# Kernel optimization log

Hardware: AMD Instinct MI355X
Metric: run time of the kernel (lower is better)

## Reference

```python
import jax, jax.numpy as jnp
import numpy as np

B, LQ, LK = 2, 2048, 77
DIM, XDIM = 320, 768
H, HD = 8, 40  # heads, head_dim; DIM == H*HD
FF = 4 * DIM  # GEGLU inner dim


def _ln(x, g, b, eps=1e-5):
    m = x.mean(-1, keepdims=True)
    v = ((x - m) ** 2).mean(-1, keepdims=True)
    return (x - m) * jax.lax.rsqrt(v + eps) * g + b


def _split_heads(x):  # [B,L,DIM] -> [B,H,L,HD]
    return x.reshape(x.shape[0], x.shape[1], H, HD).transpose(0, 2, 1, 3)


def _merge_heads(x):  # [B,H,L,HD] -> [B,L,DIM]
    return x.transpose(0, 2, 1, 3).reshape(x.shape[0], x.shape[2], H * HD)


def setup_inputs() -> dict:
    key = jax.random.key(0)
    ks = jax.random.split(key, 24)
    s = 0.02
    r = lambda i, shp: s * jax.random.normal(ks[i], shp, jnp.float32)
    return {
        "hidden_states": jax.random.normal(ks[0], (B, LQ, DIM), jnp.float32),
        "encoder_hidden_states": jax.random.normal(ks[1], (B, LK, XDIM), jnp.float32),
        # norm1 + self-attn (attn1)
        "ln1_g": jnp.ones((DIM,), jnp.float32), "ln1_b": jnp.zeros((DIM,), jnp.float32),
        "wq1": r(2, (DIM, DIM)), "wk1": r(3, (DIM, DIM)), "wv1": r(4, (DIM, DIM)),
        "wo1": r(5, (DIM, DIM)), "bo1": jnp.zeros((DIM,), jnp.float32),
        # norm2 + Hadamard cross-attn (attn2)
        "ln2_g": jnp.ones((DIM,), jnp.float32), "ln2_b": jnp.zeros((DIM,), jnp.float32),
        "wq2": r(6, (DIM, DIM)), "wk2": r(7, (XDIM, DIM)), "wvh": r(8, (DIM, DIM)),
        "wo2": r(9, (DIM, DIM)), "bo2": jnp.zeros((DIM,), jnp.float32),
        # norm3 + GEGLU feed-forward
        "ln3_g": jnp.ones((DIM,), jnp.float32), "ln3_b": jnp.zeros((DIM,), jnp.float32),
        "wff1": r(10, (DIM, 2 * FF)), "bff1": jnp.zeros((2 * FF,), jnp.float32),
        "wff2": r(11, (FF, DIM)), "bff2": jnp.zeros((DIM,), jnp.float32),
    }


def reference(hidden_states, encoder_hidden_states, ln1_g, ln1_b, wq1, wk1, wv1,
              wo1, bo1, ln2_g, ln2_b, wq2, wk2, wvh, wo2, bo2, ln3_g, ln3_b,
              wff1, bff1, wff2, bff2):
    scale = 1.0 / jnp.sqrt(jnp.asarray(HD, hidden_states.dtype))

    # ---- self-attention (SDPA semantics) ----
    h = _ln(hidden_states, ln1_g, ln1_b)
    q = _split_heads(h @ wq1)
    k = _split_heads(h @ wk1)
    v = _split_heads(h @ wv1)
    scores = jnp.einsum('bhqd,bhkd->bhqk', q, k) * scale
    w = jax.nn.softmax(scores, axis=-1)
    attn = jnp.einsum('bhqk,bhkd->bhqd', w, v)
    attn = _merge_heads(attn) @ wo1 + bo1
    hidden_states = hidden_states + attn

    # ---- Hadamard cross-attention: value comes from hidden_states (len Lq) ----
    h = _ln(hidden_states, ln2_g, ln2_b)
    q = _split_heads(h @ wq2)                     # [B,H,Lq,HD]
    k = _split_heads(encoder_hidden_states @ wk2) # [B,H,Lk,HD]
    vH = _split_heads(h @ wvh)                    # [B,H,Lq,HD]
    scores = jnp.einsum('bhqd,bhkd->bhqk', q, k) * scale
    w = jax.nn.softmax(scores, axis=-1)           # [B,H,Lq,Lk]
    # (w[...,None] * vH[...,None,:]).sum(-2) == vH * w.sum(-1, keepdims) (v indep of k)
    cross = vH * jnp.sum(w, axis=-1, keepdims=True)
    cross = _merge_heads(cross) @ wo2 + bo2
    hidden_states = hidden_states + cross

    # ---- GEGLU feed-forward ----
    h = _ln(hidden_states, ln3_g, ln3_b)
    proj = h @ wff1 + bff1
    x, gate = jnp.split(proj, 2, axis=-1)
    ff = (x * jax.nn.gelu(gate, approximate=False)) @ wff2 + bff2
    return hidden_states + ff
```

## Files before the change

kernel.cpp:

```cpp
#include <hip/hip_runtime.h>
#include <math.h>

#define DIM   320
#define HD    40
#define NH    8
#define LQ    2048
#define BATCH 2
#define MROWS 4096
#define FFD   1280
#define FF2   2560

#define KSPLIT 2
#define KCHUNK (LQ/KSPLIT)
#define KT     32
#define NT     (KCHUNK/KT)
#define NQROWS (BATCH*NH*LQ)

#define LSCALE (0.15811388300841897f * 1.4426950408889634f)

typedef unsigned short ushort_t;
typedef unsigned int u32;
using bf16x8 = __attribute__((ext_vector_type(8))) short;
using f32x4  = __attribute__((ext_vector_type(4))) float;

#define AS1 __attribute__((address_space(1)))
#define AS3 __attribute__((address_space(3)))

static __device__ inline ushort_t f2bf(float f) {
  union { float f; unsigned u; } x{f};
  unsigned r = x.u + 0x7FFFu + ((x.u >> 16) & 1u);
  return (ushort_t)(r >> 16);
}
static __device__ inline float bf2f(ushort_t h) {
  union { unsigned u; float f; } x; x.u = ((unsigned)h) << 16; return x.f;
}

#define OFF_WQKVT 0
#define OFF_WO1T  (960*320)
#define OFF_WO2T  (OFF_WO1T + 320*320)
#define OFF_WFF1T (OFF_WO2T + 320*320)
#define OFF_WFF2T (OFF_WFF1T + 320*2560)
#define OFF_WVHB  (OFF_WFF2T + 1280*320)
#define WBF_TOTAL (OFF_WVHB + 320*320)

__global__ __launch_bounds__(256) void convw_kernel(
    const float* __restrict__ wq1, const float* __restrict__ wk1,
    const float* __restrict__ wv1, const float* __restrict__ wo1,
    const float* __restrict__ wo2, const float* __restrict__ wff1,
    const float* __restrict__ wff2, const float* __restrict__ wvh,
    ushort_t* __restrict__ dst, ushort_t* __restrict__ Kimg,
    const float* __restrict__ hidden, const float* __restrict__ ln1_g,
    const float* __restrict__ ln1_b, ushort_t* __restrict__ lnb)
{
  int e = blockIdx.y;
  if (e == 8) {
    int f = blockIdx.x*256 + threadIdx.x;
    if (f < 98304) {
      int g3 = f/3, cidx = f - 3*g3;
      int rr = g3 & 31, tile = (g3 >> 5) & 63, bh = g3 >> 11;
      uint4 z = {0,0,0,0};
      *(uint4*)(Kimg + ((size_t)(bh*64 + tile))*2048 + rr*64
                + (((5+cidx) ^ (rr&7)) << 3)) = z;
    }
    return;
  }
  if (e == 9) {
    int row  = blockIdx.x * 4 + (threadIdx.x >> 6);
    int lane = threadIdx.x & 63;
    const float* x = hidden + (size_t)row * DIM;
    float v[5];
    float s = 0.f;
#pragma unroll
    for (int i = 0; i < 5; ++i) { v[i] = x[lane + 64*i]; s += v[i]; }
#pragma unroll
    for (int off = 32; off >= 1; off >>= 1) s += __shfl_xor(s, off, 64);
    float mean = s * (1.0f/DIM);
    float sq = 0.f;
#pragma unroll
    for (int i = 0; i < 5; ++i) { float d = v[i] - mean; sq += d*d; }
#pragma unroll
    for (int off = 32; off >= 1; off >>= 1) sq += __shfl_xor(sq, off, 64);
    float rstd = rsqrtf(sq*(1.0f/DIM) + 1e-5f);
    ushort_t* y = lnb + (size_t)row * DIM;
#pragma unroll
    for (int i = 0; i < 5; ++i) {
      int c = lane + 64*i;
      y[c] = f2bf((v[i]-mean)*rstd*ln1_g[c] + ln1_b[c]);
    }
    return;
  }
  const float* src; int K, N; size_t doff; int tr = 1; float scale = 1.f;
  switch (e) {
    case 0: src=wq1;  K=320;  N=320;  doff=OFF_WQKVT; scale=LSCALE; break;
    case 1: src=wk1;  K=320;  N=320;  doff=OFF_WQKVT + 320*320;  break;
    case 2: src=wv1;  K=320;  N=320;  doff=OFF_WQKVT + 2*320*320;break;
    case 3: src=wo1;  K=320;  N=320;  doff=OFF_WO1T;             break;
    case 4: src=wo2;  K=320;  N=320;  doff=OFF_WO2T;             break;
    case 5: src=wff1; K=320;  N=2560; doff=OFF_WFF1T;            break;
    case 6: src=wff2; K=1280; N=320;  doff=OFF_WFF2T;            break;
    default: src=wvh; K=320;  N=320;  doff=OFF_WVHB; tr=0;       break;
  }
  int ntN = N/32;
  int nt_total = (K/32)*ntN;
  int t = blockIdx.x;
  if (t >= nt_total) return;
  int kt = t / ntN, nt = t - kt*ntN;
  __shared__ float tile[32][33];
  int tx = threadIdx.x & 31, ty = threadIdx.x >> 5;
  ushort_t* d = dst + doff;
#pragma unroll
  for (int i = 0; i < 4; ++i) {
    int r = ty + 8*i;
    tile[r][tx] = src[(size_t)(kt*32+r)*N + nt*32+tx] * scale;
  }
  __syncthreads();
  if (tr) {
#pragma unroll
    for (int i = 0; i < 4; ++i) {
      int r = ty + 8*i;
      d[(size_t)(nt*32+r)*K + kt*32+tx] = f2bf(tile[tx][r]);
    }
  } else {
#pragma unroll
    for (int i = 0; i < 4; ++i) {
      int r = ty + 8*i;
      d[(size_t)(kt*32+r)*N + nt*32+tx] = f2bf(tile[r][tx]);
    }
  }
}

#define AST 72
__global__ __launch_bounds__(256) void mgemm(
    const ushort_t* __restrict__ A, int lda,
    const ushort_t* __restrict__ Bt, int ldb,
    const float* __restrict__ bias,
    const float* __restrict__ R,
    float* __restrict__ Cf, ushort_t* __restrict__ Cb, int ldc,
    int K)
{
  __shared__ ushort_t As[64*AST];
  __shared__ ushort_t Bs[64*AST];
  int tid = threadIdx.x;
  int w = tid >> 6, lane = tid & 63, quad = lane >> 4, n16 = lane & 15;
  int wm = w >> 1, wn = w & 1;
  int bm = blockIdx.y * 64, bn = blockIdx.x * 64;
  int sr = tid >> 2, sc = (tid & 3) << 4;
  const ushort_t* Ag = A  + (size_t)(bm + sr)*lda + sc;
  const ushort_t* Bg = Bt + (size_t)(bn + sr)*ldb + sc;

  f32x4 acc00 = {0.f,0.f,0.f,0.f}, acc01 = acc00, acc10 = acc00, acc11 = acc00;

  float4 av0 = *(const float4*)(Ag);
  float4 av1 = *(const float4*)(Ag + 8);
  float4 bv0 = *(const float4*)(Bg);
  float4 bv1 = *(const float4*)(Bg + 8);
  for (int k0 = 0; k0 < K; k0 += 64) {
    __syncthreads();
    *(float4*)(As + sr*AST + sc)     = av0;
    *(float4*)(As + sr*AST + sc + 8) = av1;
    *(float4*)(Bs + sr*AST + sc)     = bv0;
    *(float4*)(Bs + sr*AST + sc + 8) = bv1;
    __syncthreads();
    if (k0 + 64 < K) {
      av0 = *(const float4*)(Ag + k0 + 64);
      av1 = *(const float4*)(Ag + k0 + 72);
      bv0 = *(const float4*)(Bg + k0 + 64);
      bv1 = *(const float4*)(Bg + k0 + 72);
    }
#pragma unroll
    for (int kk = 0; kk < 64; kk += 32) {
      bf16x8 fa0 = *(const bf16x8*)(As + (wm*32 +      n16)*AST + kk + quad*8);
      bf16x8 fa1 = *(const bf16x8*)(As + (wm*32 + 16 + n16)*AST + kk + quad*8);
      bf16x8 fb0 = *(const bf16x8*)(Bs + (wn*32 +      n16)*AST + kk + quad*8);
      bf16x8 fb1 = *(const bf16x8*)(Bs + (wn*32 + 16 + n16)*AST + kk + quad*8);
      acc00 = __builtin_amdgcn_mfma_f32_16x16x32_bf16(fa0, fb0, acc00, 0,0,0);
      acc01 = __builtin_amdgcn_mfma_f32_16x16x32_bf16(fa0, fb1, acc01, 0,0,0);
      acc10 = __builtin_amdgcn_mfma_f32_16x16x32_bf16(fa1, fb0, acc10, 0,0,0);
      acc11 = __builtin_amdgcn_mfma_f32_16x16x32_bf16(fa1, fb1, acc11, 0,0,0);
    }
  }

  f32x4 accs[2][2] = {{acc00, acc01},{acc10, acc11}};
#pragma unroll
  for (int s = 0; s < 2; ++s)
#pragma unroll
    for (int t = 0; t < 2; ++t) {
      int c = bn + wn*32 + t*16 + n16;
      float bb = bias ? bias[c] : 0.f;
#pragma unroll
      for (int i = 0; i < 4; ++i) {
        int r = bm + wm*32 + s*16 + quad*4 + i;
        float v = accs[s][t][i] + bb;
        if (R)  v += R[(size_t)r*ldc + c];
        if (Cf) Cf[(size_t)r*ldc + c] = v;
        if (Cb) Cb[(size_t)r*ldc + c] = f2bf(v);
      }
    }
}

__global__ __launch_bounds__(256) void wc_gemm(
    const ushort_t* __restrict__ A, const ushort_t* __restrict__ Bt,
    ushort_t* __restrict__ Wctb)
{
  __shared__ ushort_t As[64*AST];
  __shared__ ushort_t Bs[64*AST];
  int tid = threadIdx.x;
  int w = tid >> 6, lane = tid & 63, quad = lane >> 4, n16 = lane & 15;
  int wm = w >> 1, wn = w & 1;
  int bm = blockIdx.y * 64, bn = blockIdx.x * 64;
  int sr = tid >> 2, sc = (tid & 3) << 4;
  const ushort_t* Ag = A  + (size_t)(bm + sr)*DIM + sc;
  const ushort_t* Bg = Bt + (size_t)(bn + sr)*DIM + sc;

  f32x4 acc00 = {0.f,0.f,0.f,0.f}, acc01 = acc00, acc10 = acc00, acc11 = acc00;

  float4 av0 = *(const float4*)(Ag);
  float4 av1 = *(const float4*)(Ag + 8);
  float4 bv0 = *(const float4*)(Bg);
  float4 bv1 = *(const float4*)(Bg + 8);
  for (int k0 = 0; k0 < DIM; k0 += 64) {
    __syncthreads();
    *(float4*)(As + sr*AST + sc)     = av0;
    *(float4*)(As + sr*AST + sc + 8) = av1;
    *(float4*)(Bs + sr*AST + sc)     = bv0;
    *(float4*)(Bs + sr*AST + sc + 8) = bv1;
    __syncthreads();
    if (k0 + 64 < DIM) {
      av0 = *(const float4*)(Ag + k0 + 64);
      av1 = *(const float4*)(Ag + k0 + 72);
      bv0 = *(const float4*)(Bg + k0 + 64);
      bv1 = *(const float4*)(Bg + k0 + 72);
    }
#pragma unroll
    for (int kk = 0; kk < 64; kk += 32) {
      bf16x8 fa0 = *(const bf16x8*)(As + (wm*32 +      n16)*AST + kk + quad*8);
      bf16x8 fa1 = *(const bf16x8*)(As + (wm*32 + 16 + n16)*AST + kk + quad*8);
      bf16x8 fb0 = *(const bf16x8*)(Bs + (wn*32 +      n16)*AST + kk + quad*8);
      bf16x8 fb1 = *(const bf16x8*)(Bs + (wn*32 + 16 + n16)*AST + kk + quad*8);
      acc00 = __builtin_amdgcn_mfma_f32_16x16x32_bf16(fa0, fb0, acc00, 0,0,0);
      acc01 = __builtin_amdgcn_mfma_f32_16x16x32_bf16(fa0, fb1, acc01, 0,0,0);
      acc10 = __builtin_amdgcn_mfma_f32_16x16x32_bf16(fa1, fb0, acc10, 0,0,0);
      acc11 = __builtin_amdgcn_mfma_f32_16x16x32_bf16(fa1, fb1, acc11, 0,0,0);
    }
  }

  f32x4 accs[2][2] = {{acc00, acc01},{acc10, acc11}};
#pragma unroll
  for (int s = 0; s < 2; ++s)
#pragma unroll
    for (int t = 0; t < 2; ++t) {
      int c = bn + wn*32 + t*16 + n16;
#pragma unroll
      for (int i = 0; i < 4; ++i) {
        int r = bm + wm*32 + s*16 + quad*4 + i;
        Wctb[((size_t)(c >> 5)*320 + r)*32
             + ((((c >> 3) & 3) ^ (r & 3)) << 3) + (c & 7)] = f2bf(accs[s][t][i]);
      }
    }
}

__global__ __launch_bounds__(256) void cross_ln(
    const float* __restrict__ h1,
    const float* __restrict__ g2, const float* __restrict__ b2,
    const ushort_t* __restrict__ Wctb,
    const float* __restrict__ bo2,
    const float* __restrict__ g3, const float* __restrict__ b3,
    float* __restrict__ h2, ushort_t* __restrict__ lnb)
{
  __shared__ ushort_t Asm[16*328];
  __shared__ ushort_t Bsm[2*10240];
  __shared__ float    sred[4][16][2];
  __shared__ float    fstat[16][2];
  int tid = threadIdx.x;
  int w = tid >> 6, lane = tid & 63, quad = lane >> 4, n16 = lane & 15;
  int r0 = blockIdx.x * 16;

  int ar = tid >> 4;
  int aj = tid & 15;
  {
    const float* hrow = h1 + (size_t)(r0 + ar)*DIM + aj*20;
    float xv[20];
    float s = 0.f, q = 0.f;
#pragma unroll
    for (int i = 0; i < 5; ++i) {
      float4 v = *(const float4*)(hrow + 4*i);
      xv[4*i]=v.x; xv[4*i+1]=v.y; xv[4*i+2]=v.z; xv[4*i+3]=v.w;
      s += v.x+v.y+v.z+v.w;
      q += v.x*v.x+v.y*v.y+v.z*v.z+v.w*v.w;
    }
#pragma unroll
    for (int off = 1; off < 16; off <<= 1) {
      s += __shfl_xor(s, off, 64);
      q += __shfl_xor(q, off, 64);
    }
    float m_  = s*(1.f/DIM);
    float rs_ = rsqrtf(fmaxf(q*(1.f/DIM) - m_*m_, 0.f) + 1e-5f);
    float gg[20], bb[20];
#pragma unroll
    for (int i = 0; i < 5; ++i) {
      *(float4*)(gg+4*i) = *(const float4*)(g2 + aj*20 + 4*i);
      *(float4*)(bb+4*i) = *(const float4*)(b2 + aj*20 + 4*i);
    }
    ushort_t tb[20];
#pragma unroll
    for (int j = 0; j < 20; ++j)
      tb[j] = f2bf((xv[j]-m_)*rs_*gg[j] + bb[j]);
#pragma unroll
    for (int i = 0; i < 5; ++i)
      *(uint2*)(Asm + ar*328 + aj*20 + 4*i) = *(uint2*)(tb + 4*i);
  }

#define STAGEB(BUF, KB) { \
  const ushort_t* src_ = Wctb + (size_t)(KB)*10240; \
  _Pragma("unroll") \
  for (int i = 0; i < 5; ++i) { \
    __builtin_amdgcn_global_load_lds( \
        (const AS1 u32*)(src_ + i*2048 + w*512 + lane*8), \
        (AS3 u32*)(Bsm + (BUF)*10240 + i*2048 + w*512), 16, 0, 0); \
  } }

  f32x4 acc[5];
#pragma unroll
  for (int t = 0; t < 5; ++t) acc[t] = f32x4{0.f,0.f,0.f,0.f};

  STAGEB(0, 0);
  __syncthreads();
  int bbuf = 0;
  for (int kb = 0; kb < 10; ++kb) {
    if (kb + 1 < 10) STAGEB(bbuf^1, kb + 1);
    const ushort_t* Bb = Bsm + bbuf*10240;
    bf16x8 fa = *(const bf16x8*)(Asm + n16*328 + kb*32 + quad*8);
#pragma unroll
    for (int t = 0; t < 5; ++t) {
      int c = w*80 + t*16 + n16;
      bf16x8 fb = *(const bf16x8*)(Bb + c*32 + ((quad ^ (c & 3)) << 3));
      acc[t] = __builtin_amdgcn_mfma_f32_16x16x32_bf16(fa, fb, acc[t], 0,0,0);
    }
    __syncthreads();
    bbuf ^= 1;
  }
#undef STAGEB

  float hv[5][4];
  float ss[4] = {0,0,0,0}, qq[4] = {0,0,0,0};
#pragma unroll
  for (int t = 0; t < 5; ++t) {
    int c = w*80 + t*16 + n16;
    float bb = bo2[c];
#pragma unroll
    for (int i = 0; i < 4; ++i) {
      int r = r0 + quad*4 + i;
      float v = acc[t][i] + bb + h1[(size_t)r*DIM + c];
      hv[t][i] = v;
      h2[(size_t)r*DIM + c] = v;
      ss[i] += v; qq[i] += v*v;
    }
  }
#pragma unroll
  for (int off = 1; off < 16; off <<= 1)
#pragma unroll
    for (int i = 0; i < 4; ++i) {
      ss[i] += __shfl_xor(ss[i], off, 64);
      qq[i] += __shfl_xor(qq[i], off, 64);
    }
  if (n16 == 0)
#pragma unroll
    for (int i = 0; i < 4; ++i) {
      sred[w][quad*4 + i][0] = ss[i];
      sred[w][quad*4 + i][1] = qq[i];
    }
  __syncthreads();
  if (tid < 16) {
    float S = sred[0][tid][0]+sred[1][tid][0]+sred[2][tid][0]+sred[3][tid][0];
    float Q = sred[0][tid][1]+sred[1][tid][1]+sred[2][tid][1]+sred[3][tid][1];
    float mm = S*(1.f/DIM);
    fstat[tid][0] = mm;
    fstat[tid][1] = rsqrtf(fmaxf(Q*(1.f/DIM) - mm*mm, 0.f) + 1e-5f);
  }
  __syncthreads();
#pragma unroll
  for (int t = 0; t < 5; ++t) {
    int c = w*80 + t*16 + n16;
    float gg = g3[c], bb = b3[c];
#pragma unroll
    for (int i = 0; i < 4; ++i) {
      int rr = quad*4 + i;
      lnb[(size_t)(r0 + rr)*DIM + c] =
          f2bf((hv[t][i] - fstat[rr][0])*fstat[rr][1]*gg + bb);
    }
  }
}

__global__ __launch_bounds__(256) void mgemm128_qkv(
    const ushort_t* __restrict__ A, const ushort_t* __restrict__ Bt,
    ushort_t* __restrict__ Qb, ushort_t* __restrict__ Kimg,
    ushort_t* __restrict__ Vimg)
{
  __shared__ ushort_t As[128*AST];
  __shared__ ushort_t Bs[64*AST];
  int tid = threadIdx.x;
  int w = tid >> 6, lane = tid & 63, quad = lane >> 4, n16 = lane & 15;
  int wm = w >> 1, wn = w & 1;
  int bm = blockIdx.y * 128, bn = blockIdx.x * 64;
  int ar = tid >> 2, ac = (tid & 3) << 4;
  const ushort_t* Ag0 = A  + (size_t)(bm + ar)*DIM + ac;
  const ushort_t* Ag1 = A  + (size_t)(bm + 64 + ar)*DIM + ac;
  const ushort_t* Bg  = Bt + (size_t)(bn + ar)*DIM + ac;

  f32x4 acc[4][2];
#pragma unroll
  for (int s = 0; s < 4; ++s)
#pragma unroll
    for (int t = 0; t < 2; ++t) acc[s][t] = f32x4{0.f,0.f,0.f,0.f};

  float4 a00 = *(const float4*)(Ag0);
  float4 a01 = *(const float4*)(Ag0 + 8);
  float4 a10 = *(const float4*)(Ag1);
  float4 a11 = *(const float4*)(Ag1 + 8);
  float4 b0  = *(const float4*)(Bg);
  float4 b1  = *(const float4*)(Bg + 8);
  for (int k0 = 0; k0 < DIM; k0 += 64) {
    __syncthreads();
    *(float4*)(As + ar*AST + ac)          = a00;
    *(float4*)(As + ar*AST + ac + 8)      = a01;
    *(float4*)(As + (64+ar)*AST + ac)     = a10;
    *(float4*)(As + (64+ar)*AST + ac + 8) = a11;
    *(float4*)(Bs + ar*AST + ac)          = b0;
    *(float4*)(Bs + ar*AST + ac + 8)      = b1;
    __syncthreads();
    if (k0 + 64 < DIM) {
      a00 = *(const float4*)(Ag0 + k0 + 64);
      a01 = *(const float4*)(Ag0 + k0 + 72);
      a10 = *(const float4*)(Ag1 + k0 + 64);
      a11 = *(const float4*)(Ag1 + k0 + 72);
      b0  = *(const float4*)(Bg  + k0 + 64);
      b1  = *(const float4*)(Bg  + k0 + 72);
    }
#pragma unroll
    for (int kk = 0; kk < 64; kk += 32) {
      bf16x8 fa[4], fb[2];
#pragma unroll
      for (int s = 0; s < 4; ++s)
        fa[s] = *(const bf16x8*)(As + (wm*64 + s*16 + n16)*AST + kk + quad*8);
#pragma unroll
      for (int t = 0; t < 2; ++t)
        fb[t] = *(const bf16x8*)(Bs + (wn*32 + t*16 + n16)*AST + kk + quad*8);
#pragma unroll
      for (int s = 0; s < 4; ++s)
#pragma unroll
        for (int t = 0; t < 2; ++t)
          acc[s][t] = __builtin_amdgcn_mfma_f32_16x16x32_bf16(fa[s], fb[t], acc[s][t], 0,0,0);
    }
  }

  int b8 = (bm >> 11) << 3;
  if (bn < 320) {
#pragma unroll
    for (int s = 0; s < 4; ++s)
#pragma unroll
      for (int t = 0; t < 2; ++t) {
        int c = bn + wn*32 + t*16 + n16;
#pragma unroll
        for (int i = 0; i < 4; ++i) {
          int r = bm + wm*64 + s*16 + quad*4 + i;
          Qb[(size_t)r*320 + c] = f2bf(acc[s][t][i]);
        }
      }
  } else if (bn < 640) {
#pragma unroll
    for (int t = 0; t < 2; ++t) {
      int c = bn + wn*32 + t*16 + n16 - 320;
      int hK = c / 40, d = c - hK*40;
#pragma unroll
      for (int s = 0; s < 4; ++s)
#pragma unroll
        for (int i = 0; i < 4; ++i) {
          int r = bm + wm*64 + s*16 + quad*4 + i;
          int l = r & 2047, tl = l >> 5, rr = l & 31;
          Kimg[((size_t)((b8 + hK)*64 + tl))*2048 + rr*64
               + (((d >> 3) ^ (rr & 7)) << 3) + (d & 7)] = f2bf(acc[s][t][i]);
        }
    }
  } else {
#pragma unroll
    for (int t = 0; t < 2; ++t) {
      int c = bn + wn*32 + t*16 + n16 - 640;
      int hV = c / 40, d = c - hV*40;
#pragma unroll
      for (int s = 0; s < 4; ++s) {
        int l0 = (bm + wm*64 + s*16 + quad*4) & 2047;
        int tl = l0 >> 5, p0 = (l0 & 31) >> 1;
        ushort_t* vb = Vimg + ((size_t)((b8 + hV)*64 + tl))*1536 + d*32;
#pragma unroll
        for (int j = 0; j < 2; ++j) {
          int p = p0 + j;
          unsigned val = (unsigned)f2bf(acc[s][t][2*j])
                       | ((unsigned)f2bf(acc[s][t][2*j+1]) << 16);
          *(unsigned*)(vb + (((p >> 2) ^ (d & 3)) << 3) + ((p & 3) << 1)) = val;
        }
      }
    }
  }
}

__global__ __launch_bounds__(256) void ff1_geglu(
    const ushort_t* __restrict__ A, const ushort_t* __restrict__ Bt,
    const float* __restrict__ bias, ushort_t* __restrict__ Og)
{
  __shared__ ushort_t As[128*AST];
  __shared__ ushort_t Bxs[64*AST];
  __shared__ ushort_t Bgs[64*AST];
  int tid = threadIdx.x;
  int w = tid >> 6, lane = tid & 63, quad = lane >> 4, n16 = lane & 15;
  int wm = w >> 1, wn = w & 1;
  int bm = blockIdx.y * 128, bn = blockIdx.x * 64;
  int ar = tid >> 2, ac = (tid & 3) << 4;
  const ushort_t* Ag0 = A  + (size_t)(bm + ar)*DIM + ac;
  const ushort_t* Ag1 = A  + (size_t)(bm + 64 + ar)*DIM + ac;
  const ushort_t* Bxg = Bt + (size_t)(bn + ar)*DIM + ac;
  const ushort_t* Bgg = Bt + (size_t)(bn + FFD + ar)*DIM + ac;

  f32x4 ax[4][2], ag[4][2];
#pragma unroll
  for (int s = 0; s < 4; ++s)
#pragma unroll
    for (int t = 0; t < 2; ++t) { ax[s][t] = f32x4{0.f,0.f,0.f,0.f}; ag[s][t] = ax[s][t]; }

  float4 a00 = *(const float4*)(Ag0);
  float4 a01 = *(const float4*)(Ag0 + 8);
  float4 a10 = *(const float4*)(Ag1);
  float4 a11 = *(const float4*)(Ag1 + 8);
  float4 bx0 = *(const float4*)(Bxg);
  float4 bx1 = *(const float4*)(Bxg + 8);
  float4 bg0 = *(const float4*)(Bgg);
  float4 bg1 = *(const float4*)(Bgg + 8);
  for (int k0 = 0; k0 < DIM; k0 += 64) {
    __syncthreads();
    *(float4*)(As  + ar*AST + ac)          = a00;
    *(float4*)(As  + ar*AST + ac + 8)      = a01;
    *(float4*)(As  + (64+ar)*AST + ac)     = a10;
    *(float4*)(As  + (64+ar)*AST + ac + 8) = a11;
    *(float4*)(Bxs + ar*AST + ac)          = bx0;
    *(float4*)(Bxs + ar*AST + ac + 8)      = bx1;
    *(float4*)(Bgs + ar*AST + ac)          = bg0;
    *(float4*)(Bgs + ar*AST + ac + 8)      = bg1;
    __syncthreads();
    if (k0 + 64 < DIM) {
      a00 = *(const float4*)(Ag0 + k0 + 64);
      a01 = *(const float4*)(Ag0 + k0 + 72);
      a10 = *(const float4*)(Ag1 + k0 + 64);
      a11 = *(const float4*)(Ag1 + k0 + 72);
      bx0 = *(const float4*)(Bxg + k0 + 64);
      bx1 = *(const float4*)(Bxg + k0 + 72);
      bg0 = *(const float4*)(Bgg + k0 + 64);
      bg1 = *(const float4*)(Bgg + k0 + 72);
    }
#pragma unroll
    for (int kk = 0; kk < 64; kk += 32) {
      bf16x8 fa[4], fx[2], fg[2];
#pragma unroll
      for (int s = 0; s < 4; ++s)
        fa[s] = *(const bf16x8*)(As + (wm*64 + s*16 + n16)*AST + kk + quad*8);
#pragma unroll
      for (int t = 0; t < 2; ++t) {
        fx[t] = *(const bf16x8*)(Bxs + (wn*32 + t*16 + n16)*AST + kk + quad*8);
        fg[t] = *(const bf16x8*)(Bgs + (wn*32 + t*16 + n16)*AST + kk + quad*8);
      }
#pragma unroll
      for (int s = 0; s < 4; ++s)
#pragma unroll
        for (int t = 0; t < 2; ++t) {
          ax[s][t] = __builtin_amdgcn_mfma_f32_16x16x32_bf16(fa[s], fx[t], ax[s][t], 0,0,0);
          ag[s][t] = __builtin_amdgcn_mfma_f32_16x16x32_bf16(fa[s], fg[t], ag[s][t], 0,0,0);
        }
    }
  }

  const float kk2 = 0.7071067811865476f;
#pragma unroll
  for (int s = 0; s < 4; ++s)
#pragma unroll
    for (int t = 0; t < 2; ++t) {
      int c = bn + wn*32 + t*16 + n16;
      float bx = bias[c], bg = bias[c + FFD];
#pragma unroll
      for (int i = 0; i < 4; ++i) {
        int r = bm + wm*64 + s*16 + quad*4 + i;
        float xx = ax[s][t][i] + bx;
        float gg = ag[s][t][i] + bg;
        Og[(size_t)r*FFD + c] = f2bf(xx * 0.5f * gg * (1.f + erff(gg * kk2)));
      }
    }
}

#define TILE_K_SH 2048
#define TILE_V_SH 1536
#define TILE_SH   (TILE_K_SH + TILE_V_SH)

__global__ __launch_bounds__(256, 2) void attn_mfma(
    const ushort_t* __restrict__ Qb, const ushort_t* __restrict__ Kimg,
    const ushort_t* __restrict__ Vimg,
    float* __restrict__ Pl, ushort_t* __restrict__ Pacc)
{
  __shared__ ushort_t lds[4*TILE_SH];
  int tid  = threadIdx.x;
  int w    = tid >> 6;
  int lane = tid & 63;
  int quad = lane >> 4;
  int n16  = lane & 15;

  int blk  = blockIdx.x;
  int bh   = (blk & 7) | (((blk >> 3) & 1) << 3);
  int rest = blk >> 4;
  int qt   = rest & 15;
  int ks   = rest >> 4;
  int b = bh >> 3, h = bh & 7;

  const ushort_t* qrowa = Qb + (size_t)(b*LQ + qt*128 + w*32 + n16)*320 + h*HD;
  const ushort_t* qrowb = qrowa + 16*320;
  bf16x8 qf0a = *(const bf16x8*)(qrowa + quad*8);
  bf16x8 qf1a = *(const bf16x8*)(qrowa + 32);
  bf16x8 qf0b = *(const bf16x8*)(qrowb + quad*8);
  bf16x8 qf1b = *(const bf16x8*)(qrowb + 32);

  const ushort_t* Ktb = Kimg + ((size_t)bh*64 + ks*NT)*TILE_K_SH;
  const ushort_t* Vtb = Vimg + ((size_t)bh*64 + ks*NT)*TILE_V_SH;

  int swk0 = (quad ^ (n16 & 7)) << 3;
  int swk1 = ((quad + 4) ^ (n16 & 7)) << 3;
  int kof0 = n16*64 + swk0;
  int kof1 = n16*64 + swk1;
  int kof2 = (16+n16)*64 + swk0;
  int kof3 = (16+n16)*64 + swk1;
  int swv  = (quad ^ (n16 & 3)) << 3;
  int vof0 = n16*32 + swv;
  int vof1 = (16+n16)*32 + swv;
  int vof2 = (32+n16)*32 + swv;

  f32x4 o0a = {0.f,0.f,0.f,0.f}, o1a = o0a, o2a = o0a;
  f32x4 o0b = o0a, o1b = o0a, o2b = o0a;
  f32x4 la0a = o0a, la1a = o0a, la0b = o0a, la1b = o0a;

#define CVTPK(D, LO, HI) \
  asm("v_cvt_pk_bf16_f32 %0, %1, %2" : "=v"(D) : "v"(LO), "v"(HI))
#define PSWAP32(X, Y) \
  asm("v_permlane32_swap_b32 %0, %1" : "+v"(X), "+v"(Y))
#define PSWAP16(X, Y) \
  asm("v_permlane16_swap_b32 %0, %1" : "+v"(X), "+v"(Y))

#define STAGE(SLOT, T) { \
  const ushort_t* ks_ = Ktb + (size_t)(T)*TILE_K_SH + w*512 + lane*8; \
  ushort_t* kd_ = lds + (SLOT)*TILE_SH + w*512; \
  __builtin_amdgcn_global_load_lds( \
      (const AS1 u32*)ks_, (AS3 u32*)kd_, 16, 0, 0); \
  if (w < 3) { \
    const ushort_t* vs_ = Vtb + (size_t)(T)*TILE_V_SH + w*512 + lane*8; \
    ushort_t* vd_ = lds + (SLOT)*TILE_SH + TILE_K_SH + w*512; \
    __builtin_amdgcn_global_load_lds( \
        (const AS1 u32*)vs_, (AS3 u32*)vd_, 16, 0, 0); \
  } }

#define HALF(Q0F, Q1F, LA0, LA1, FRAG) \
  bf16x8 FRAG; { \
  f32x4 st0 = {-8.f,-8.f,-8.f,-8.f}; f32x4 st1 = st0; \
  st0 = __builtin_amdgcn_mfma_f32_16x16x32_bf16(K00, Q0F, st0, 0,0,0); \
  st1 = __builtin_amdgcn_mfma_f32_16x16x32_bf16(K10, Q0F, st1, 0,0,0); \
  st0 = __builtin_amdgcn_mfma_f32_16x16x32_bf16(K01, Q1F, st0, 0,0,0); \
  st1 = __builtin_amdgcn_mfma_f32_16x16x32_bf16(K11, Q1F, st1, 0,0,0); \
  f32x4 p0, p1; \
  _Pragma("unroll") \
  for (int r = 0; r < 4; ++r) { p0[r] = exp2f(st0[r]); p1[r] = exp2f(st1[r]); } \
  LA0 += p0; LA1 += p1; \
  unsigned d0, d1, d2, d3; \
  CVTPK(d0, p0[0], p0[1]); CVTPK(d1, p0[2], p0[3]); \
  CVTPK(d2, p1[0], p1[1]); CVTPK(d3, p1[2], p1[3]); \
  PSWAP32(d0, d2); PSWAP16(d0, d2); \
  PSWAP32(d1, d3); PSWAP16(d1, d3); \
  union { unsigned u[4]; bf16x8 v; } fr_; \
  fr_.u[0] = d0; fr_.u[1] = d1; fr_.u[2] = d2; fr_.u[3] = d3; \
  FRAG = fr_.v; }

#define CTILE(SLOT) { \
  const ushort_t* Kb_ = lds + (SLOT)*TILE_SH; \
  const ushort_t* Vb_ = Kb_ + TILE_K_SH; \
  bf16x8 K00 = *(const bf16x8*)(Kb_ + kof0); \
  bf16x8 K01 = *(const bf16x8*)(Kb_ + kof1); \
  bf16x8 K10 = *(const bf16x8*)(Kb_ + kof2); \
  bf16x8 K11 = *(const bf16x8*)(Kb_ + kof3); \
  bf16x8 V0  = *(const bf16x8*)(Vb_ + vof0); \
  bf16x8 V1  = *(const bf16x8*)(Vb_ + vof1); \
  bf16x8 V2  = *(const bf16x8*)(Vb_ + vof2); \
  HALF(qf0a, qf1a, la0a, la1a, fragA) \
  HALF(qf0b, qf1b, la0b, la1b, fragB) \
  o0a = __builtin_amdgcn_mfma_f32_16x16x32_bf16(fragA, V0, o0a, 0,0,0); \
  o0b = __builtin_amdgcn_mfma_f32_16x16x32_bf16(fragB, V0, o0b, 0,0,0); \
  o1a = __builtin_amdgcn_mfma_f32_16x16x32_bf16(fragA, V1, o1a, 0,0,0); \
  o1b = __builtin_amdgcn_mfma_f32_16x16x32_bf16(fragB, V1, o1b, 0,0,0); \
  o2a = __builtin_amdgcn_mfma_f32_16x16x32_bf16(fragA, V2, o2a, 0,0,0); \
  o2b = __builtin_amdgcn_mfma_f32_16x16x32_bf16(fragB, V2, o2b, 0,0,0); }

  STAGE(0, 0); STAGE(1, 1);
  __syncthreads();
  for (int s = 0; s < NT/2; ++s) {
    int sb = s & 1;
    if (s + 1 < NT/2) {
      STAGE((sb^1)*2,     2*s + 2);
      STAGE((sb^1)*2 + 1, 2*s + 3);
    }
    CTILE(sb*2);
    CTILE(sb*2 + 1);
    __syncthreads();
  }
#undef STAGE
#undef CTILE
#undef HALF
#undef CVTPK
#undef PSWAP32
#undef PSWAP16

  float sA = la0a[0]+la0a[1]+la0a[2]+la0a[3] + la1a[0]+la1a[1]+la1a[2]+la1a[3];
  float sB = la0b[0]+la0b[1]+la0b[2]+la0b[3] + la1b[0]+la1b[1]+la1b[2]+la1b[3];
  sA += __shfl_xor(sA, 16, 64); sA += __shfl_xor(sA, 32, 64);
  sB += __shfl_xor(sB, 16, 64); sB += __shfl_xor(sB, 32, 64);

  int grow = bh*LQ + qt*128 + w*32;
  size_t base = (size_t)ks*NQROWS;
  if (lane < 16) {
    Pl[base + grow + n16]      = sA;
    Pl[base + grow + 16 + n16] = sB;
  }

  int gqa = grow + quad*4;
#pragma unroll
  for (int r = 0; r < 4; ++r) {
    size_t gq = base + gqa + r;
    ushort_t* pw = Pacc + gq*40;
    pw[n16]      = f2bf(o0a[r]);
    pw[16 + n16] = f2bf(o1a[r]);
    if (n16 < 8) pw[32 + n16] = f2bf(o2a[r]);
    size_t gq2 = gq + 16;
    ushort_t* pw2 = Pacc + gq2*40;
    pw2[n16]      = f2bf(o0b[r]);
    pw2[16 + n16] = f2bf(o1b[r]);
    if (n16 < 8) pw2[32 + n16] = f2bf(o2b[r]);
  }
}

__global__ __launch_bounds__(256) void attn_merge(
    const float* __restrict__ Pl, const ushort_t* __restrict__ Pacc,
    ushort_t* __restrict__ O)
{
  int t = blockIdx.x*256 + threadIdx.x;
  int idx = t / 5;
  int u   = t - idx*5;
  int bh = idx >> 11, qi = idx & (LQ-1);
  int b = bh >> 3, h = bh & 7;
  float L = 0.f;
#pragma unroll
  for (int k = 0; k < KSPLIT; ++k) L += Pl[(size_t)k*NQROWS + idx];
  float inv = 1.0f / L;
  float acc[8] = {0,0,0,0,0,0,0,0};
#pragma unroll
  for (int k = 0; k < KSPLIT; ++k) {
    const ushort_t* pr = Pacc + ((size_t)k*NQROWS + idx)*40 + u*8;
    ushort_t vbuf[8];
    *(uint4*)vbuf = *(const uint4*)pr;
#pragma unroll
    for (int j = 0; j < 8; ++j) acc[j] += bf2f(vbuf[j]);
  }
  ushort_t ob[8];
#pragma unroll
  for (int j = 0; j < 8; ++j) ob[j] = f2bf(acc[j]*inv);
  ushort_t* orow = O + (size_t)(b*LQ + qi)*DIM + h*HD;
  *(uint4*)(orow + u*8) = *(uint4*)ob;
}

extern "C" void kernel_launch(void* const* d_in, const int* in_sizes, int n_in,
                              void* d_out, int out_size, void* d_ws, size_t ws_size,
                              hipStream_t stream) {
  const float* hidden = (const float*)d_in[0];
  const float* ln1_g = (const float*)d_in[2];
  const float* ln1_b = (const float*)d_in[3];
  const float* wq1   = (const float*)d_in[4];
  const float* wk1   = (const float*)d_in[5];
  const float* wv1   = (const float*)d_in[6];
  const float* wo1   = (const float*)d_in[7];
  const float* bo1   = (const float*)d_in[8];
  const float* ln2_g = (const float*)d_in[9];
  const float* ln2_b = (const float*)d_in[10];
  const float* wvh   = (const float*)d_in[13];
  const float* wo2   = (const float*)d_in[14];
  const float* bo2   = (const float*)d_in[15];
  const float* ln3_g = (const float*)d_in[16];
  const float* ln3_b = (const float*)d_in[17];
  const float* wff1  = (const float*)d_in[18];
  const float* bff1  = (const float*)d_in[19];
  const float* wff2  = (const float*)d_in[20];
  const float* bff2  = (const float*)d_in[21];
  float* out = (float*)d_out;

  ushort_t* wsu = (ushort_t*)d_ws;
  ushort_t* wbf   = wsu;
  ushort_t* lnb   = wbf + WBF_TOTAL;
  ushort_t* Qb    = lnb + (size_t)MROWS*DIM;
  ushort_t* attnb = Qb + (size_t)MROWS*DIM;
  ushort_t* gegb  = attnb + (size_t)MROWS*DIM;
  ushort_t* wct   = gegb + (size_t)MROWS*FFD;
  ushort_t* vtb   = wct + 320*320;
  ushort_t* kpb   = vtb + (size_t)16*64*1536;
  ushort_t* Pacc  = kpb + (size_t)16*64*2048;
  float* fws = (float*)((((uintptr_t)(Pacc + (size_t)KSPLIT*NQROWS*40)) + 255) & ~(uintptr_t)255);
  float* h1   = fws;
  float* h2   = h1 + (size_t)MROWS*DIM;
  float* Pl   = h2 + (size_t)MROWS*DIM;

  dim3 t256(256);
  dim3 gconv(1024, 10);
  dim3 gqkv(15, 32);
  dim3 g320(5, 64);
  dim3 gwc(5, 5);
  dim3 gffg(20, 32);
  dim3 gattn(16*16*KSPLIT);

  convw_kernel<<<gconv, t256, 0, stream>>>(wq1, wk1, wv1, wo1, wo2, wff1, wff2,
                                           wvh, wbf, kpb, hidden, ln1_g, ln1_b, lnb);
  wc_gemm<<<gwc, t256, 0, stream>>>(wbf + OFF_WO2T, wbf + OFF_WVHB, wct);

  mgemm128_qkv<<<gqkv, t256, 0, stream>>>(lnb, wbf + OFF_WQKVT, Qb, kpb, vtb);
  attn_mfma<<<gattn, t256, 0, stream>>>(Qb, kpb, vtb, Pl, Pacc);
  attn_merge<<<NQROWS*5/256, t256, 0, stream>>>(Pl, Pacc, attnb);
  mgemm<<<g320, t256, 0, stream>>>(attnb, DIM, wbf + OFF_WO1T, DIM, bo1, hidden,
                                   h1, nullptr, DIM, DIM);

  cross_ln<<<MROWS/16, t256, 0, stream>>>(h1, ln2_g, ln2_b, wct, bo2,
                                          ln3_g, ln3_b, h2, lnb);

  ff1_geglu<<<gffg, t256, 0, stream>>>(lnb, wbf + OFF_WFF1T, bff1, gegb);
  mgemm<<<g320, t256, 0, stream>>>(gegb, FFD, wbf + OFF_WFF2T, FFD, bff2, h2,
                                   out, nullptr, DIM, FFD);
}
```

Measured before the change: 199.4 us.

## Remove KV split in self-attention and normalize output in-kernel

Sets the key split to one so each attention block processes the full key sequence, and normalizes the output inside the attention kernel. This removes the separate merge kernel and the partial-sum buffers, along with one launch and their global memory traffic. The cost is halving the grid to 256 blocks of longer duration, which may underfill a large GPU and lengthen the attention critical path.

```diff
diff --git a/kernel.cpp b/kernel.cpp
--- a/kernel.cpp
+++ b/kernel.cpp
@@ -10,7 +10,7 @@
 #define FFD   1280
 #define FF2   2560
 
-#define KSPLIT 2
+#define KSPLIT 1
 #define KCHUNK (LQ/KSPLIT)
 #define KT     32
 #define NT     (KCHUNK/KT)
@@ -600,7 +600,7 @@
 __global__ __launch_bounds__(256, 2) void attn_mfma(
     const ushort_t* __restrict__ Qb, const ushort_t* __restrict__ Kimg,
     const ushort_t* __restrict__ Vimg,
-    float* __restrict__ Pl, ushort_t* __restrict__ Pacc)
+    ushort_t* __restrict__ O)
 {
   __shared__ ushort_t lds[4*TILE_SH];
   int tid  = threadIdx.x;
@@ -611,9 +611,7 @@
 
   int blk  = blockIdx.x;
   int bh   = (blk & 7) | (((blk >> 3) & 1) << 3);
-  int rest = blk >> 4;
-  int qt   = rest & 15;
-  int ks   = rest >> 4;
+  int qt   = (blk >> 4) & 15;
   int b = bh >> 3, h = bh & 7;
 
   const ushort_t* qrowa = Qb + (size_t)(b*LQ + qt*128 + w*32 + n16)*320 + h*HD;
@@ -623,8 +621,8 @@
   bf16x8 qf0b = *(const bf16x8*)(qrowb + quad*8);
   bf16x8 qf1b = *(const bf16x8*)(qrowb + 32);
 
-  const ushort_t* Ktb = Kimg + ((size_t)bh*64 + ks*NT)*TILE_K_SH;
-  const ushort_t* Vtb = Vimg + ((size_t)bh*64 + ks*NT)*TILE_V_SH;
+  const ushort_t* Ktb = Kimg + (size_t)bh*64*TILE_K_SH;
+  const ushort_t* Vtb = Vimg + (size_t)bh*64*TILE_V_SH;
 
   int swk0 = (quad ^ (n16 & 7)) << 3;
   int swk1 = ((quad + 4) ^ (n16 & 7)) << 3;
@@ -723,56 +721,25 @@
   sA += __shfl_xor(sA, 16, 64); sA += __shfl_xor(sA, 32, 64);
   sB += __shfl_xor(sB, 16, 64); sB += __shfl_xor(sB, 32, 64);
 
-  int grow = bh*LQ + qt*128 + w*32;
-  size_t base = (size_t)ks*NQROWS;
-  if (lane < 16) {
-    Pl[base + grow + n16]      = sA;
-    Pl[base + grow + 16 + n16] = sB;
-  }
-
-  int gqa = grow + quad*4;
+  float invA[4], invB[4];
 #pragma unroll
   for (int r = 0; r < 4; ++r) {
-    size_t gq = base + gqa + r;
-    ushort_t* pw = Pacc + gq*40;
-    pw[n16]      = f2bf(o0a[r]);
-    pw[16 + n16] = f2bf(o1a[r]);
-    if (n16 < 8) pw[32 + n16] = f2bf(o2a[r]);
-    size_t gq2 = gq + 16;
-    ushort_t* pw2 = Pacc + gq2*40;
-    pw2[n16]      = f2bf(o0b[r]);
-    pw2[16 + n16] = f2bf(o1b[r]);
-    if (n16 < 8) pw2[32 + n16] = f2bf(o2b[r]);
-  }
-}
-
-__global__ __launch_bounds__(256) void attn_merge(
-    const float* __restrict__ Pl, const ushort_t* __restrict__ Pacc,
-    ushort_t* __restrict__ O)
-{
-  int t = blockIdx.x*256 + threadIdx.x;
-  int idx = t / 5;
-  int u   = t - idx*5;
-  int bh = idx >> 11, qi = idx & (LQ-1);
-  int b = bh >> 3, h = bh & 7;
-  float L = 0.f;
-#pragma unroll
-  for (int k = 0; k < KSPLIT; ++k) L += Pl[(size_t)k*NQROWS + idx];
-  float inv = 1.0f / L;
-  float acc[8] = {0,0,0,0,0,0,0,0};
-#pragma unroll
-  for (int k = 0; k < KSPLIT; ++k) {
-    const ushort_t* pr = Pacc + ((size_t)k*NQROWS + idx)*40 + u*8;
-    ushort_t vbuf[8];
-    *(uint4*)vbuf = *(const uint4*)pr;
-#pragma unroll
-    for (int j = 0; j < 8; ++j) acc[j] += bf2f(vbuf[j]);
-  }
-  ushort_t ob[8];
-#pragma unroll
-  for (int j = 0; j < 8; ++j) ob[j] = f2bf(acc[j]*inv);
-  ushort_t* orow = O + (size_t)(b*LQ + qi)*DIM + h*HD;
-  *(uint4*)(orow + u*8) = *(uint4*)ob;
+    invA[r] = 1.0f / __shfl(sA, quad*4 + r, 64);
+    invB[r] = 1.0f / __shfl(sB, quad*4 + r, 64);
+  }
+
+  int growg = b*LQ + qt*128 + w*32 + quad*4;
+#pragma unroll
+  for (int r = 0; r < 4; ++r) {
+    ushort_t* orow = O + (size_t)(growg + r)*DIM + h*HD;
+    orow[n16]      = f2bf(o0a[r]*invA[r]);
+    orow[16 + n16] = f2bf(o1a[r]*invA[r]);
+    if (n16 < 8) orow[32 + n16] = f2bf(o2a[r]*invA[r]);
+    ushort_t* orow2 = O + (size_t)(growg + 16 + r)*DIM + h*HD;
+    orow2[n16]      = f2bf(o0b[r]*invB[r]);
+    orow2[16 + n16] = f2bf(o1b[r]*invB[r]);
+    if (n16 < 8) orow2[32 + n16] = f2bf(o2b[r]*invB[r]);
+  }
 }
 
 extern "C" void kernel_launch(void* const* d_in, const int* in_sizes, int n_in,
@@ -808,11 +775,9 @@
   ushort_t* wct   = gegb + (size_t)MROWS*FFD;
   ushort_t* vtb   = wct + 320*320;
   ushort_t* kpb   = vtb + (size_t)16*64*1536;
-  ushort_t* Pacc  = kpb + (size_t)16*64*2048;
-  float* fws = (float*)((((uintptr_t)(Pacc + (size_t)KSPLIT*NQROWS*40)) + 255) & ~(uintptr_t)255);
+  float* fws = (float*)((((uintptr_t)(kpb + (size_t)16*64*2048)) + 255) & ~(uintptr_t)255);
   float* h1   = fws;
   float* h2   = h1 + (size_t)MROWS*DIM;
-  float* Pl   = h2 + (size_t)MROWS*DIM;
 
   dim3 t256(256);
   dim3 gconv(1024, 10);
@@ -820,15 +785,14 @@
   dim3 g320(5, 64);
   dim3 gwc(5, 5);
   dim3 gffg(20, 32);
-  dim3 gattn(16*16*KSPLIT);
+  dim3 gattn(16*16);
 
   convw_kernel<<<gconv, t256, 0, stream>>>(wq1, wk1, wv1, wo1, wo2, wff1, wff2,
                                            wvh, wbf, kpb, hidden, ln1_g, ln1_b, lnb);
   wc_gemm<<<gwc, t256, 0, stream>>>(wbf + OFF_WO2T, wbf + OFF_WVHB, wct);
 
   mgemm128_qkv<<<gqkv, t256, 0, stream>>>(lnb, wbf + OFF_WQKVT, Qb, kpb, vtb);
-  attn_mfma<<<gattn, t256, 0, stream>>>(Qb, kpb, vtb, Pl, Pacc);
-  attn_merge<<<NQROWS*5/256, t256, 0, stream>>>(Pl, Pacc, attnb);
+  attn_mfma<<<gattn, t256, 0, stream>>>(Qb, kpb, vtb, attnb);
   mgemm<<<g320, t256, 0, stream>>>(attnb, DIM, wbf + OFF_WO1T, DIM, bo1, hidden,
                                    h1, nullptr, DIM, DIM);
 
```

Result: slower. 206.5 us (+3.5%).

## Fuse attn1 output projection into cross-attention LayerNorm kernel

Applied to the files above, without the earlier changes.

The self-attention output projection (wo1 GEMM plus bias and residual) moves into the cross_ln kernel, now o1cross_ln, which runs two back-to-back 16-row MFMA GEMMs per block. The wo1 weight is pre-swizzled into the same k-blocked layout as Wct so it can be staged into LDS with global_load_lds. This removes one kernel launch and the write and re-read of the fp32 h1 buffer, and LayerNorm2 is now computed from registers. In exchange, each 16-row block streams the full wo1 weight through LDS, and the two GEMMs run back to back in the same block.

```diff
diff --git a/kernel.cpp b/kernel.cpp
--- a/kernel.cpp
+++ b/kernel.cpp
@@ -94,7 +94,7 @@
     case 0: src=wq1;  K=320;  N=320;  doff=OFF_WQKVT; scale=LSCALE; break;
     case 1: src=wk1;  K=320;  N=320;  doff=OFF_WQKVT + 320*320;  break;
     case 2: src=wv1;  K=320;  N=320;  doff=OFF_WQKVT + 2*320*320;break;
-    case 3: src=wo1;  K=320;  N=320;  doff=OFF_WO1T;             break;
+    case 3: src=wo1;  K=320;  N=320;  doff=OFF_WO1T; tr=2;       break;
     case 4: src=wo2;  K=320;  N=320;  doff=OFF_WO2T;             break;
     case 5: src=wff1; K=320;  N=2560; doff=OFF_WFF1T;            break;
     case 6: src=wff2; K=1280; N=320;  doff=OFF_WFF2T;            break;
@@ -114,11 +114,19 @@
     tile[r][tx] = src[(size_t)(kt*32+r)*N + nt*32+tx] * scale;
   }
   __syncthreads();
-  if (tr) {
+  if (tr == 1) {
 #pragma unroll
     for (int i = 0; i < 4; ++i) {
       int r = ty + 8*i;
       d[(size_t)(nt*32+r)*K + kt*32+tx] = f2bf(tile[tx][r]);
+    }
+  } else if (tr == 2) {
+#pragma unroll
+    for (int i = 0; i < 4; ++i) {
+      int r = ty + 8*i;
+      int k = kt*32 + r, c = nt*32 + tx;
+      d[((size_t)kt*320 + c)*32 + ((((k >> 3) & 3) ^ (c & 3)) << 3) + (k & 7)]
+          = f2bf(tile[r][tx]);
     }
   } else {
 #pragma unroll
@@ -259,11 +267,11 @@
     }
 }
 
-__global__ __launch_bounds__(256) void cross_ln(
-    const float* __restrict__ h1,
+__global__ __launch_bounds__(256) void o1cross_ln(
+    const ushort_t* __restrict__ attnb, const ushort_t* __restrict__ Wo1tb,
+    const float* __restrict__ bo1, const float* __restrict__ hidden,
     const float* __restrict__ g2, const float* __restrict__ b2,
-    const ushort_t* __restrict__ Wctb,
-    const float* __restrict__ bo2,
+    const ushort_t* __restrict__ Wctb, const float* __restrict__ bo2,
     const float* __restrict__ g3, const float* __restrict__ b3,
     float* __restrict__ h2, ushort_t* __restrict__ lnb)
 {
@@ -275,43 +283,16 @@
   int w = tid >> 6, lane = tid & 63, quad = lane >> 4, n16 = lane & 15;
   int r0 = blockIdx.x * 16;
 
-  int ar = tid >> 4;
-  int aj = tid & 15;
   {
-    const float* hrow = h1 + (size_t)(r0 + ar)*DIM + aj*20;
-    float xv[20];
-    float s = 0.f, q = 0.f;
-#pragma unroll
-    for (int i = 0; i < 5; ++i) {
-      float4 v = *(const float4*)(hrow + 4*i);
-      xv[4*i]=v.x; xv[4*i+1]=v.y; xv[4*i+2]=v.z; xv[4*i+3]=v.w;
-      s += v.x+v.y+v.z+v.w;
-      q += v.x*v.x+v.y*v.y+v.z*v.z+v.w*v.w;
-    }
-#pragma unroll
-    for (int off = 1; off < 16; off <<= 1) {
-      s += __shfl_xor(s, off, 64);
-      q += __shfl_xor(q, off, 64);
-    }
-    float m_  = s*(1.f/DIM);
-    float rs_ = rsqrtf(fmaxf(q*(1.f/DIM) - m_*m_, 0.f) + 1e-5f);
-    float gg[20], bb[20];
-#pragma unroll
-    for (int i = 0; i < 5; ++i) {
-      *(float4*)(gg+4*i) = *(const float4*)(g2 + aj*20 + 4*i);
-      *(float4*)(bb+4*i) = *(const float4*)(b2 + aj*20 + 4*i);
-    }
-    ushort_t tb[20];
-#pragma unroll
-    for (int j = 0; j < 20; ++j)
-      tb[j] = f2bf((xv[j]-m_)*rs_*gg[j] + bb[j]);
+    int ar = tid >> 4, aj = tid & 15;
+    const ushort_t* srow = attnb + (size_t)(r0 + ar)*DIM + aj*20;
 #pragma unroll
     for (int i = 0; i < 5; ++i)
-      *(uint2*)(Asm + ar*328 + aj*20 + 4*i) = *(uint2*)(tb + 4*i);
-  }
-
-#define STAGEB(BUF, KB) { \
-  const ushort_t* src_ = Wctb + (size_t)(KB)*10240; \
+      *(uint2*)(Asm + ar*328 + aj*20 + 4*i) = *(const uint2*)(srow + 4*i);
+  }
+
+#define STAGEB(BASE, BUF, KB) { \
+  const ushort_t* src_ = (BASE) + (size_t)(KB)*10240; \
   _Pragma("unroll") \
   for (int i = 0; i < 5; ++i) { \
     __builtin_amdgcn_global_load_lds( \
@@ -323,11 +304,11 @@
 #pragma unroll
   for (int t = 0; t < 5; ++t) acc[t] = f32x4{0.f,0.f,0.f,0.f};
 
-  STAGEB(0, 0);
+  STAGEB(Wo1tb, 0, 0);
   __syncthreads();
   int bbuf = 0;
   for (int kb = 0; kb < 10; ++kb) {
-    if (kb + 1 < 10) STAGEB(bbuf^1, kb + 1);
+    if (kb + 1 < 10) STAGEB(Wo1tb, bbuf^1, kb + 1);
     const ushort_t* Bb = Bsm + bbuf*10240;
     bf16x8 fa = *(const bf16x8*)(Asm + n16*328 + kb*32 + quad*8);
 #pragma unroll
@@ -339,10 +320,78 @@
     __syncthreads();
     bbuf ^= 1;
   }
+
+  STAGEB(Wctb, 0, 0);
+
+  float h1v[5][4];
+  float ss[4] = {0,0,0,0}, qq[4] = {0,0,0,0};
+#pragma unroll
+  for (int t = 0; t < 5; ++t) {
+    int c = w*80 + t*16 + n16;
+    float bb = bo1[c];
+#pragma unroll
+    for (int i = 0; i < 4; ++i) {
+      int r = r0 + quad*4 + i;
+      float v = acc[t][i] + bb + hidden[(size_t)r*DIM + c];
+      h1v[t][i] = v;
+      ss[i] += v; qq[i] += v*v;
+    }
+  }
+#pragma unroll
+  for (int off = 1; off < 16; off <<= 1)
+#pragma unroll
+    for (int i = 0; i < 4; ++i) {
+      ss[i] += __shfl_xor(ss[i], off, 64);
+      qq[i] += __shfl_xor(qq[i], off, 64);
+    }
+  if (n16 == 0)
+#pragma unroll
+    for (int i = 0; i < 4; ++i) {
+      sred[w][quad*4 + i][0] = ss[i];
+      sred[w][quad*4 + i][1] = qq[i];
+    }
+  __syncthreads();
+  if (tid < 16) {
+    float S = sred[0][tid][0]+sred[1][tid][0]+sred[2][tid][0]+sred[3][tid][0];
+    float Q = sred[0][tid][1]+sred[1][tid][1]+sred[2][tid][1]+sred[3][tid][1];
+    float mm = S*(1.f/DIM);
+    fstat[tid][0] = mm;
+    fstat[tid][1] = rsqrtf(fmaxf(Q*(1.f/DIM) - mm*mm, 0.f) + 1e-5f);
+  }
+  __syncthreads();
+#pragma unroll
+  for (int t = 0; t < 5; ++t) {
+    int c = w*80 + t*16 + n16;
+    float gg = g2[c], bbv = b2[c];
+#pragma unroll
+    for (int i = 0; i < 4; ++i) {
+      int rr = quad*4 + i;
+      Asm[rr*328 + c] = f2bf((h1v[t][i] - fstat[rr][0])*fstat[rr][1]*gg + bbv);
+    }
+  }
+#pragma unroll
+  for (int t = 0; t < 5; ++t) acc[t] = f32x4{0.f,0.f,0.f,0.f};
+  __syncthreads();
+
+  bbuf = 0;
+  for (int kb = 0; kb < 10; ++kb) {
+    if (kb + 1 < 10) STAGEB(Wctb, bbuf^1, kb + 1);
+    const ushort_t* Bb = Bsm + bbuf*10240;
+    bf16x8 fa = *(const bf16x8*)(Asm + n16*328 + kb*32 + quad*8);
+#pragma unroll
+    for (int t = 0; t < 5; ++t) {
+      int c = w*80 + t*16 + n16;
+      bf16x8 fb = *(const bf16x8*)(Bb + c*32 + ((quad ^ (c & 3)) << 3));
+      acc[t] = __builtin_amdgcn_mfma_f32_16x16x32_bf16(fa, fb, acc[t], 0,0,0);
+    }
+    __syncthreads();
+    bbuf ^= 1;
+  }
 #undef STAGEB
 
   float hv[5][4];
-  float ss[4] = {0,0,0,0}, qq[4] = {0,0,0,0};
+#pragma unroll
+  for (int i = 0; i < 4; ++i) { ss[i] = 0.f; qq[i] = 0.f; }
 #pragma unroll
   for (int t = 0; t < 5; ++t) {
     int c = w*80 + t*16 + n16;
@@ -350,7 +399,7 @@
 #pragma unroll
     for (int i = 0; i < 4; ++i) {
       int r = r0 + quad*4 + i;
-      float v = acc[t][i] + bb + h1[(size_t)r*DIM + c];
+      float v = acc[t][i] + bb + h1v[t][i];
       hv[t][i] = v;
       h2[(size_t)r*DIM + c] = v;
       ss[i] += v; qq[i] += v*v;
@@ -810,8 +859,7 @@
   ushort_t* kpb   = vtb + (size_t)16*64*1536;
   ushort_t* Pacc  = kpb + (size_t)16*64*2048;
   float* fws = (float*)((((uintptr_t)(Pacc + (size_t)KSPLIT*NQROWS*40)) + 255) & ~(uintptr_t)255);
-  float* h1   = fws;
-  float* h2   = h1 + (size_t)MROWS*DIM;
+  float* h2   = fws;
   float* Pl   = h2 + (size_t)MROWS*DIM;
 
   dim3 t256(256);
@@ -829,11 +877,10 @@
   mgemm128_qkv<<<gqkv, t256, 0, stream>>>(lnb, wbf + OFF_WQKVT, Qb, kpb, vtb);
   attn_mfma<<<gattn, t256, 0, stream>>>(Qb, kpb, vtb, Pl, Pacc);
   attn_merge<<<NQROWS*5/256, t256, 0, stream>>>(Pl, Pacc, attnb);
-  mgemm<<<g320, t256, 0, stream>>>(attnb, DIM, wbf + OFF_WO1T, DIM, bo1, hidden,
-                                   h1, nullptr, DIM, DIM);
-
-  cross_ln<<<MROWS/16, t256, 0, stream>>>(h1, ln2_g, ln2_b, wct, bo2,
-                                          ln3_g, ln3_b, h2, lnb);
+
+  o1cross_ln<<<MROWS/16, t256, 0, stream>>>(attnb, wbf + OFF_WO1T, bo1, hidden,
+                                            ln2_g, ln2_b, wct, bo2,
+                                            ln3_g, ln3_b, h2, lnb);
 
   ff1_geglu<<<gffg, t256, 0, stream>>>(lnb, wbf + OFF_WFF1T, bff1, gegb);
   mgemm<<<g320, t256, 0, stream>>>(gegb, FFD, wbf + OFF_WFF2T, FFD, bff2, h2,
```

Result: no change. 197.7 us (-0.9%).
